# Performance work log

Hardware: AMD Instinct MI355X
Metric: run time of the kernel (lower is better)

Reference implementation:

```python
import jax, jax.numpy as jnp
import numpy as np

N_NODES = 50000
N_EDGES = 800000
IN_F = 256
OUT_F = 128
ALPHA = 0.2  # LeakyReLU negative slope


def setup_inputs() -> dict:
    key = jax.random.key(0)
    k_h, k_row, k_col, k_W, k_a = jax.random.split(key, 5)
    h = jax.random.normal(k_h, (N_NODES, IN_F), dtype=jnp.float32)
    row = jax.random.randint(k_row, (N_EDGES,), 0, N_NODES)
    # Guarantee every node appears as a destination so unique(dst) == arange(N)
    col = jnp.concatenate([
        jnp.arange(N_NODES),
        jax.random.randint(k_col, (N_EDGES - N_NODES,), 0, N_NODES),
    ])
    adj = jnp.stack([row, col]).astype(jnp.int64)
    # Xavier-uniform-ish params (gain 1.414)
    lim_W = 1.414 * np.sqrt(6.0 / (IN_F + OUT_F))
    W = jax.random.uniform(k_W, (IN_F, OUT_F), minval=-lim_W, maxval=lim_W, dtype=jnp.float32)
    lim_a = 1.414 * np.sqrt(6.0 / (2 * OUT_F + 1))
    a = jax.random.uniform(k_a, (2 * OUT_F, 1), minval=-lim_a, maxval=lim_a, dtype=jnp.float32)
    return {"h": h, "adj": adj, "W": W, "a": a}


def reference(h, adj, W, a):
    N = h.shape[0]
    self_loops = jnp.arange(N)  # == unique(adj[1]) by input construction
    row = jnp.concatenate([adj[0], self_loops])  # [E_total]
    col = jnp.concatenate([adj[1], self_loops])  # [E_total]

    Wh = h @ W                                    # [N, OUT_F]
    s_src = (Wh @ a[:OUT_F]).squeeze(-1)          # [N] (Wh1)
    s_dst = (Wh @ a[OUT_F:]).squeeze(-1)          # [N] (Wh2)

    e = jax.nn.leaky_relu(s_dst[col] + s_src[row], negative_slope=ALPHA)  # [E_total]

    # segment softmax over destination nodes
    e_max = jax.ops.segment_max(e, col, num_segments=N)
    ex = jnp.exp(e - e_max[col])
    denom = jax.ops.segment_sum(ex, col, num_segments=N)
    att = ex / denom[col]                         # [E_total]

    h_prime = jax.ops.segment_sum(Wh[row] * att[:, None], col, num_segments=N)  # [N, OUT_F]
    return jax.nn.elu(h_prime)  # concat=True
```

## Files before the change

### kernel.cpp

```cpp
#include <hip/hip_runtime.h>
#include <math.h>

#define N_NODES 50000
#define N_EDGES 800000
#define E_TOTAL (N_NODES + N_EDGES)
#define IN_F 256
#define OUT_F 128
#define ALPHA 0.2f

#define GEMM_WAVES ((N_NODES + 31) / 32)
#define GEMM_BLOCKS ((GEMM_WAVES + 3) / 4)
#define LINK_BLOCKS ((N_EDGES + 255) / 256)
#define NODE_BLOCKS ((N_NODES + 255) / 256)

typedef short bf16x8 __attribute__((ext_vector_type(8)));
typedef float f32x4  __attribute__((ext_vector_type(4)));

static __device__ __forceinline__ unsigned short f2bf(float f) {
    unsigned int u = __float_as_uint(f);
    u += 0x7FFFu + ((u >> 16) & 1u);
    return (unsigned short)(u >> 16);
}
static __device__ __forceinline__ float bf2f(unsigned int u16) {
    return __uint_as_float(u16 << 16);
}

__global__ __launch_bounds__(256) void k_prep(const float* __restrict__ W,
                                              const float* __restrict__ a,
                                              int* __restrict__ head,
                                              int* __restrict__ cnt,
                                              int* __restrict__ total,
                                              float* __restrict__ Wa,
                                              unsigned short* __restrict__ WbT) {
    const int b = blockIdx.x, t = threadIdx.x;
    if (b < NODE_BLOCKS) {
        int i = b * 256 + t;
        if (i < N_NODES) { head[i] = -1; cnt[i] = 1; }
    } else if (b == NODE_BLOCKS) {
        if (t == 0) *total = 0;
        const int k = t;
        const float4* wr  = (const float4*)(W + (size_t)k * OUT_F);
        const float4* av1 = (const float4*)a;
        const float4* av2 = (const float4*)(a + OUT_F);
        float s1 = 0.0f, s2 = 0.0f;
#pragma unroll 8
        for (int i = 0; i < OUT_F / 4; ++i) {
            float4 w = wr[i], x = av1[i], y = av2[i];
            s1 = fmaf(w.x, x.x, fmaf(w.y, x.y, fmaf(w.z, x.z, fmaf(w.w, x.w, s1))));
            s2 = fmaf(w.x, y.x, fmaf(w.y, y.y, fmaf(w.z, y.z, fmaf(w.w, y.w, s2))));
        }
        Wa[k] = s1;
        Wa[IN_F + k] = s2;
    } else {
        const int n = b - (NODE_BLOCKS + 1);
        WbT[(size_t)n * IN_F + t] = f2bf(W[(size_t)t * OUT_F + n]);
    }
}

__global__ __launch_bounds__(256) void k_gemm_link(const float* __restrict__ h,
                                                   const unsigned short* __restrict__ WbT,
                                                   const float* __restrict__ Wa,
                                                   const int* __restrict__ adj,
                                                   unsigned short* __restrict__ Whb,
                                                   float* __restrict__ s_src,
                                                   float* __restrict__ s_dst,
                                                   int* __restrict__ head,
                                                   int* __restrict__ cnt,
                                                   int2* __restrict__ list) {
    if (blockIdx.x >= GEMM_BLOCKS) {
        int e = (blockIdx.x - GEMM_BLOCKS) * 256 + threadIdx.x;
        if (e >= N_EDGES) return;
        int src = adj[e];
        int col = adj[N_EDGES + e];
        int old = atomicExch(&head[col], e);
        list[e] = make_int2(src, old);
        atomicAdd(&cnt[col], 1);
        return;
    }
    const int wid  = blockIdx.x * 4 + (threadIdx.x >> 6);
    const int lane = threadIdx.x & 63;
    if (wid >= GEMM_WAVES) return;
    const int m = lane & 15, grp = lane >> 4;
    const int row0 = wid * 32;

    f32x4 acc[2][8];
#pragma unroll
    for (int rt = 0; rt < 2; ++rt)
#pragma unroll
        for (int nt = 0; nt < 8; ++nt) acc[rt][nt] = (f32x4){0.f, 0.f, 0.f, 0.f};
    float sp1[2] = {0.f, 0.f}, sp2[2] = {0.f, 0.f};

    for (int kt = 0; kt < 8; ++kt) {
        const int k0 = kt * 32;
        bf16x8 hfrag[2];
#pragma unroll
        for (int rt = 0; rt < 2; ++rt) {
            int r = row0 + rt * 16 + m;
            if (r >= N_NODES) r = N_NODES - 1;
            const float4* hp = (const float4*)(h + (size_t)r * IN_F + k0 + grp * 8);
            float4 x0 = hp[0], x1 = hp[1];
            const float4* wap1 = (const float4*)(Wa + k0 + grp * 8);
            const float4* wap2 = (const float4*)(Wa + IN_F + k0 + grp * 8);
            float4 a0 = wap1[0], a1 = wap1[1];
            float4 b0 = wap2[0], b1 = wap2[1];
            sp1[rt] = fmaf(x0.x, a0.x, fmaf(x0.y, a0.y, fmaf(x0.z, a0.z, fmaf(x0.w, a0.w, sp1[rt]))));
            sp1[rt] = fmaf(x1.x, a1.x, fmaf(x1.y, a1.y, fmaf(x1.z, a1.z, fmaf(x1.w, a1.w, sp1[rt]))));
            sp2[rt] = fmaf(x0.x, b0.x, fmaf(x0.y, b0.y, fmaf(x0.z, b0.z, fmaf(x0.w, b0.w, sp2[rt]))));
            sp2[rt] = fmaf(x1.x, b1.x, fmaf(x1.y, b1.y, fmaf(x1.z, b1.z, fmaf(x1.w, b1.w, sp2[rt]))));
            bf16x8 hf;
            hf[0] = (short)f2bf(x0.x); hf[1] = (short)f2bf(x0.y);
            hf[2] = (short)f2bf(x0.z); hf[3] = (short)f2bf(x0.w);
            hf[4] = (short)f2bf(x1.x); hf[5] = (short)f2bf(x1.y);
            hf[6] = (short)f2bf(x1.z); hf[7] = (short)f2bf(x1.w);
            hfrag[rt] = hf;
        }
#pragma unroll
        for (int nt = 0; nt < 8; ++nt) {
            bf16x8 wf = *(const bf16x8*)(WbT + (size_t)(nt * 16 + m) * IN_F + k0 + grp * 8);
            acc[0][nt] = __builtin_amdgcn_mfma_f32_16x16x32_bf16(wf, hfrag[0], acc[0][nt], 0, 0, 0);
            acc[1][nt] = __builtin_amdgcn_mfma_f32_16x16x32_bf16(wf, hfrag[1], acc[1][nt], 0, 0, 0);
        }
    }

#pragma unroll
    for (int rt = 0; rt < 2; ++rt) {
        const int row = row0 + rt * 16 + m;
        const bool valid = (row < N_NODES);
        float t1 = sp1[rt], t2 = sp2[rt];
        t1 += __shfl_xor(t1, 16); t1 += __shfl_xor(t1, 32);
        t2 += __shfl_xor(t2, 16); t2 += __shfl_xor(t2, 32);
        if (valid && grp == 0) { s_src[row] = t1; s_dst[row] = t2; }
        if (valid) {
            unsigned short* orow = Whb + (size_t)row * OUT_F;
#pragma unroll
            for (int nt = 0; nt < 8; ++nt) {
                f32x4 v = acc[rt][nt];
                ushort4 pk;
                pk.x = f2bf(v[0]); pk.y = f2bf(v[1]);
                pk.z = f2bf(v[2]); pk.w = f2bf(v[3]);
                *(ushort4*)(orow + nt * 16 + grp * 4) = pk;
            }
        }
    }
}

__global__ __launch_bounds__(256) void k_offsets(const int* __restrict__ cnt,
                                                 int* __restrict__ start,
                                                 int* __restrict__ total) {
    int i = blockIdx.x * blockDim.x + threadIdx.x;
    if (i >= N_NODES) return;
    start[i] = atomicAdd(total, cnt[i]);
}

__global__ __launch_bounds__(256) void k_walk(const int* __restrict__ head,
                                              const int2* __restrict__ list,
                                              const float* __restrict__ s_src,
                                              const float* __restrict__ s_dst,
                                              const int* __restrict__ start,
                                              int2* __restrict__ pack,
                                              float* __restrict__ denom) {
    int node = blockIdx.x * blockDim.x + threadIdx.x;
    if (node >= N_NODES) return;
    float sd = s_dst[node];
    int p = start[node];

    float s0 = sd + s_src[node];
    float lr0 = (s0 > 0.0f) ? s0 : ALPHA * s0;
    float x0 = __expf(lr0);
    pack[p++] = make_int2(node, __float_as_int(x0));
    float dsum = x0;

    int e = head[node];
    while (e >= 0) {
        int2 rec = list[e];
        e = rec.y;
        float ss = s_src[rec.x];
        float s = sd + ss;
        float lr = (s > 0.0f) ? s : ALPHA * s;
        float x = __expf(lr);
        pack[p++] = make_int2(rec.x, __float_as_int(x));
        dsum += x;
    }
    denom[node] = dsum;
}

__global__ __launch_bounds__(256) void k_gather(const unsigned short* __restrict__ Whb,
                                                const int* __restrict__ start,
                                                const int* __restrict__ cnt,
                                                const int2* __restrict__ pack,
                                                const float* __restrict__ denom,
                                                float* __restrict__ out) {
    int node = (blockIdx.x * blockDim.x + threadIdx.x) >> 6;
    int lane = threadIdx.x & 63;
    if (node >= N_NODES) return;
    int s0 = start[node];
    int n  = cnt[node];
    const uint* __restrict__ Wv = (const uint*)Whb;

    float ax = 0.0f, ay = 0.0f;
    int j = 0;
    for (; j + 8 <= n; j += 8) {
        int2 p0 = pack[s0 + j + 0];
        int2 p1 = pack[s0 + j + 1];
        int2 p2 = pack[s0 + j + 2];
        int2 p3 = pack[s0 + j + 3];
        int2 p4 = pack[s0 + j + 4];
        int2 p5 = pack[s0 + j + 5];
        int2 p6 = pack[s0 + j + 6];
        int2 p7 = pack[s0 + j + 7];
        uint w0 = Wv[(size_t)p0.x * (OUT_F / 2) + lane];
        uint w1 = Wv[(size_t)p1.x * (OUT_F / 2) + lane];
        uint w2 = Wv[(size_t)p2.x * (OUT_F / 2) + lane];
        uint w3 = Wv[(size_t)p3.x * (OUT_F / 2) + lane];
        uint w4 = Wv[(size_t)p4.x * (OUT_F / 2) + lane];
        uint w5 = Wv[(size_t)p5.x * (OUT_F / 2) + lane];
        uint w6 = Wv[(size_t)p6.x * (OUT_F / 2) + lane];
        uint w7 = Wv[(size_t)p7.x * (OUT_F / 2) + lane];
        float x0 = __int_as_float(p0.y), x1 = __int_as_float(p1.y);
        float x2 = __int_as_float(p2.y), x3 = __int_as_float(p3.y);
        float x4 = __int_as_float(p4.y), x5 = __int_as_float(p5.y);
        float x6 = __int_as_float(p6.y), x7 = __int_as_float(p7.y);
        ax = fmaf(x0, bf2f(w0 & 0xFFFFu), ax); ay = fmaf(x0, bf2f(w0 >> 16), ay);
        ax = fmaf(x1, bf2f(w1 & 0xFFFFu), ax); ay = fmaf(x1, bf2f(w1 >> 16), ay);
        ax = fmaf(x2, bf2f(w2 & 0xFFFFu), ax); ay = fmaf(x2, bf2f(w2 >> 16), ay);
        ax = fmaf(x3, bf2f(w3 & 0xFFFFu), ax); ay = fmaf(x3, bf2f(w3 >> 16), ay);
        ax = fmaf(x4, bf2f(w4 & 0xFFFFu), ax); ay = fmaf(x4, bf2f(w4 >> 16), ay);
        ax = fmaf(x5, bf2f(w5 & 0xFFFFu), ax); ay = fmaf(x5, bf2f(w5 >> 16), ay);
        ax = fmaf(x6, bf2f(w6 & 0xFFFFu), ax); ay = fmaf(x6, bf2f(w6 >> 16), ay);
        ax = fmaf(x7, bf2f(w7 & 0xFFFFu), ax); ay = fmaf(x7, bf2f(w7 >> 16), ay);
    }
    for (; j < n; ++j) {
        int2 p = pack[s0 + j];
        uint w = Wv[(size_t)p.x * (OUT_F / 2) + lane];
        float x = __int_as_float(p.y);
        ax = fmaf(x, bf2f(w & 0xFFFFu), ax);
        ay = fmaf(x, bf2f(w >> 16), ay);
    }
    float inv = 1.0f / denom[node];
    float vx = ax * inv;
    float vy = ay * inv;
    vx = (vx > 0.0f) ? vx : expm1f(vx);
    vy = (vy > 0.0f) ? vy : expm1f(vy);
    ((float2*)(out + (size_t)node * OUT_F))[lane] = make_float2(vx, vy);
}

extern "C" void kernel_launch(void* const* d_in, const int* in_sizes, int n_in,
                              void* d_out, int out_size, void* d_ws, size_t ws_size,
                              hipStream_t stream) {
    const float* h   = (const float*)d_in[0];
    const int*   adj = (const int*)d_in[1];
    const float* W   = (const float*)d_in[2];
    const float* a   = (const float*)d_in[3];
    float* out = (float*)d_out;

    char* ws = (char*)d_ws;
    const size_t SZ_WHB = (size_t)N_NODES * OUT_F * 2;
    const size_t SZ_N   = 200704;
    const size_t SZ_E8  = (size_t)N_EDGES * 8;
    unsigned short* Whb = (unsigned short*)(ws);
    float* s_src   = (float*)(ws + SZ_WHB);
    float* s_dst   = (float*)(ws + SZ_WHB + SZ_N);
    int*   head    = (int*)  (ws + SZ_WHB + 2 * SZ_N);
    int*   cnt     = (int*)  (ws + SZ_WHB + 3 * SZ_N);
    int*   start   = (int*)  (ws + SZ_WHB + 4 * SZ_N);
    float* denom   = (float*)(ws + SZ_WHB + 5 * SZ_N);
    int*   total   = (int*)  (ws + SZ_WHB + 6 * SZ_N);
    float* Wa      = (float*)(ws + SZ_WHB + 6 * SZ_N + 256);
    unsigned short* WbT = (unsigned short*)(ws + SZ_WHB + 6 * SZ_N + 256 + 2048);
    int2*  list    = (int2*) (ws + SZ_WHB + 6 * SZ_N + 256 + 2048 + 65536);
    int2*  pack    = (int2*) (ws + SZ_WHB + 6 * SZ_N + 256 + 2048 + 65536 + SZ_E8);

    (void)in_sizes; (void)n_in; (void)out_size; (void)ws_size;

    k_prep     <<<NODE_BLOCKS + 1 + OUT_F, 256, 0, stream>>>(W, a, head, cnt, total, Wa, WbT);
    k_gemm_link<<<GEMM_BLOCKS + LINK_BLOCKS, 256, 0, stream>>>(h, WbT, Wa, adj, Whb,
                                                               s_src, s_dst, head, cnt, list);
    k_offsets  <<<NODE_BLOCKS, 256, 0, stream>>>(cnt, start, total);
    k_walk     <<<NODE_BLOCKS, 256, 0, stream>>>(head, list, s_src, s_dst, start, pack, denom);
    k_gather   <<<(N_NODES * 64 + 255) / 256, 256, 0, stream>>>(Whb, start, cnt, pack, denom, out);
}
```

Baseline: 235.9 us.

## Replace per-edge count atomics with list-walk counting and wave-level prefix scan

```diff
diff --git a/kernel.cpp b/kernel.cpp
--- a/kernel.cpp
+++ b/kernel.cpp
@@ -10,7 +10,6 @@
 
 #define GEMM_WAVES ((N_NODES + 31) / 32)
 #define GEMM_BLOCKS ((GEMM_WAVES + 3) / 4)
-#define LINK_BLOCKS ((N_EDGES + 255) / 256)
 #define NODE_BLOCKS ((N_NODES + 255) / 256)
 
 typedef short bf16x8 __attribute__((ext_vector_type(8)));
@@ -28,14 +27,13 @@
 __global__ __launch_bounds__(256) void k_prep(const float* __restrict__ W,
                                               const float* __restrict__ a,
                                               int* __restrict__ head,
-                                              int* __restrict__ cnt,
                                               int* __restrict__ total,
                                               float* __restrict__ Wa,
                                               unsigned short* __restrict__ WbT) {
     const int b = blockIdx.x, t = threadIdx.x;
     if (b < NODE_BLOCKS) {
         int i = b * 256 + t;
-        if (i < N_NODES) { head[i] = -1; cnt[i] = 1; }
+        if (i < N_NODES) head[i] = -1;
     } else if (b == NODE_BLOCKS) {
         if (t == 0) *total = 0;
         const int k = t;
@@ -57,27 +55,13 @@
     }
 }
 
-__global__ __launch_bounds__(256) void k_gemm_link(const float* __restrict__ h,
-                                                   const unsigned short* __restrict__ WbT,
-                                                   const float* __restrict__ Wa,
-                                                   const int* __restrict__ adj,
-                                                   unsigned short* __restrict__ Whb,
-                                                   float* __restrict__ s_src,
-                                                   float* __restrict__ s_dst,
-                                                   int* __restrict__ head,
-                                                   int* __restrict__ cnt,
-                                                   int2* __restrict__ list) {
-    if (blockIdx.x >= GEMM_BLOCKS) {
-        int e = (blockIdx.x - GEMM_BLOCKS) * 256 + threadIdx.x;
-        if (e >= N_EDGES) return;
-        int src = adj[e];
-        int col = adj[N_EDGES + e];
-        int old = atomicExch(&head[col], e);
-        list[e] = make_int2(src, old);
-        atomicAdd(&cnt[col], 1);
-        return;
-    }
-    const int wid  = blockIdx.x * 4 + (threadIdx.x >> 6);
+__global__ __launch_bounds__(256) void k_gemm(const float* __restrict__ h,
+                                              const unsigned short* __restrict__ WbT,
+                                              const float* __restrict__ Wa,
+                                              unsigned short* __restrict__ Whb,
+                                              float* __restrict__ s_src,
+                                              float* __restrict__ s_dst) {
+    const int wid  = (blockIdx.x * blockDim.x + threadIdx.x) >> 6;
     const int lane = threadIdx.x & 63;
     if (wid >= GEMM_WAVES) return;
     const int m = lane & 15, grp = lane >> 4;
@@ -144,57 +128,87 @@
     }
 }
 
-__global__ __launch_bounds__(256) void k_offsets(const int* __restrict__ cnt,
-                                                 int* __restrict__ start,
-                                                 int* __restrict__ total) {
-    int i = blockIdx.x * blockDim.x + threadIdx.x;
-    if (i >= N_NODES) return;
-    start[i] = atomicAdd(total, cnt[i]);
+__global__ __launch_bounds__(256) void k_link(const int* __restrict__ adj,
+                                              int* __restrict__ head,
+                                              int2* __restrict__ list) {
+    int e = blockIdx.x * blockDim.x + threadIdx.x;
+    if (e >= N_EDGES) return;
+    int src = adj[e];
+    int col = adj[N_EDGES + e];
+    int old = atomicExch(&head[col], e);
+    list[e] = make_int2(src, old);
 }
 
 __global__ __launch_bounds__(256) void k_walk(const int* __restrict__ head,
                                               const int2* __restrict__ list,
                                               const float* __restrict__ s_src,
                                               const float* __restrict__ s_dst,
-                                              const int* __restrict__ start,
+                                              int* __restrict__ total,
+                                              int* __restrict__ startA,
+                                              int* __restrict__ cntA,
                                               int2* __restrict__ pack,
                                               float* __restrict__ denom) {
-    int node = blockIdx.x * blockDim.x + threadIdx.x;
-    if (node >= N_NODES) return;
+    const int node = blockIdx.x * blockDim.x + threadIdx.x;
+    const int lane = threadIdx.x & 63;
+    const bool active = (node < N_NODES);
+
+    int myCnt = 0;
+    int e0 = -1;
+    if (active) {
+        myCnt = 1;
+        e0 = head[node];
+        int e = e0;
+        while (e >= 0) { e = list[e].y; ++myCnt; }
+    }
+
+    int x = myCnt;
+#pragma unroll
+    for (int off = 1; off < 64; off <<= 1) {
+        int y = __shfl_up(x, off);
+        if (lane >= off) x += y;
+    }
+    int excl = x - myCnt;
+    int wtot = __shfl(x, 63);
+    int base = 0;
+    if (lane == 0) base = atomicAdd(total, wtot);
+    base = __shfl(base, 0);
+    int p = base + excl;
+
+    if (!active) return;
+    startA[node] = p;
+    cntA[node]   = myCnt;
+
     float sd = s_dst[node];
-    int p = start[node];
-
     float s0 = sd + s_src[node];
     float lr0 = (s0 > 0.0f) ? s0 : ALPHA * s0;
     float x0 = __expf(lr0);
     pack[p++] = make_int2(node, __float_as_int(x0));
     float dsum = x0;
 
-    int e = head[node];
+    int e = e0;
     while (e >= 0) {
         int2 rec = list[e];
         e = rec.y;
-        float ss = s_src[rec.x];
-        float s = sd + ss;
+        float s = sd + s_src[rec.x];
         float lr = (s > 0.0f) ? s : ALPHA * s;
-        float x = __expf(lr);
-        pack[p++] = make_int2(rec.x, __float_as_int(x));
-        dsum += x;
+        float ex = __expf(lr);
+        pack[p++] = make_int2(rec.x, __float_as_int(ex));
+        dsum += ex;
     }
     denom[node] = dsum;
 }
 
 __global__ __launch_bounds__(256) void k_gather(const unsigned short* __restrict__ Whb,
-                                                const int* __restrict__ start,
-                                                const int* __restrict__ cnt,
+                                                const int* __restrict__ startA,
+                                                const int* __restrict__ cntA,
                                                 const int2* __restrict__ pack,
                                                 const float* __restrict__ denom,
                                                 float* __restrict__ out) {
     int node = (blockIdx.x * blockDim.x + threadIdx.x) >> 6;
     int lane = threadIdx.x & 63;
     if (node >= N_NODES) return;
-    int s0 = start[node];
-    int n  = cnt[node];
+    int s0 = startA[node];
+    int n  = cntA[node];
     const uint* __restrict__ Wv = (const uint*)Whb;
 
     float ax = 0.0f, ay = 0.0f;
@@ -261,8 +275,8 @@
     float* s_src   = (float*)(ws + SZ_WHB);
     float* s_dst   = (float*)(ws + SZ_WHB + SZ_N);
     int*   head    = (int*)  (ws + SZ_WHB + 2 * SZ_N);
-    int*   cnt     = (int*)  (ws + SZ_WHB + 3 * SZ_N);
-    int*   start   = (int*)  (ws + SZ_WHB + 4 * SZ_N);
+    int*   startA  = (int*)  (ws + SZ_WHB + 3 * SZ_N);
+    int*   cntA    = (int*)  (ws + SZ_WHB + 4 * SZ_N);
     float* denom   = (float*)(ws + SZ_WHB + 5 * SZ_N);
     int*   total   = (int*)  (ws + SZ_WHB + 6 * SZ_N);
     float* Wa      = (float*)(ws + SZ_WHB + 6 * SZ_N + 256);
@@ -272,10 +286,11 @@
 
     (void)in_sizes; (void)n_in; (void)out_size; (void)ws_size;
 
-    k_prep     <<<NODE_BLOCKS + 1 + OUT_F, 256, 0, stream>>>(W, a, head, cnt, total, Wa, WbT);
-    k_gemm_link<<<GEMM_BLOCKS + LINK_BLOCKS, 256, 0, stream>>>(h, WbT, Wa, adj, Whb,
-                                                               s_src, s_dst, head, cnt, list);
-    k_offsets  <<<NODE_BLOCKS, 256, 0, stream>>>(cnt, start, total);
-    k_walk     <<<NODE_BLOCKS, 256, 0, stream>>>(head, list, s_src, s_dst, start, pack, denom);
-    k_gather   <<<(N_NODES * 64 + 255) / 256, 256, 0, stream>>>(Whb, start, cnt, pack, denom, out);
-}
+    k_prep  <<<NODE_BLOCKS + 1 + OUT_F, 256, 0, stream>>>(W, a, head, total, Wa, WbT);
+    k_gemm  <<<GEMM_BLOCKS, 256, 0, stream>>>(h, WbT, Wa, Whb, s_src, s_dst);
+    k_link  <<<(N_EDGES + 255) / 256, 256, 0, stream>>>(adj, head, list);
+    k_walk  <<<NODE_BLOCKS, 256, 0, stream>>>(head, list, s_src, s_dst, total,
+                                              startA, cntA, pack, denom);
+    k_gather<<<(N_NODES * 64 + 255) / 256, 256, 0, stream>>>(Whb, startA, cntA,
+                                                             pack, denom, out);
+}
```

After: 236.5 us. Within noise of the previous version (+0.2%).
